# Optimization experiments

Measured on AMD Instinct MI355X. Metric: run time of the kernel, lower is better.

## Reference

```python
import jax, jax.numpy as jnp
import numpy as np

N = 100000   # nodes
E = 1600000  # directed edges
HID = 64


def gat_conv(x, src, dst, W, a_src, a_dst, b, heads, out_ch):
    """PyG-style GATConv (add_self_loops=True, negative_slope=0.2, concat)."""
    n = x.shape[0]
    h = (x @ W).reshape(n, heads, out_ch)              # [N,H,C]
    loop = jnp.arange(n, dtype=src.dtype)
    s = jnp.concatenate([src, loop])                   # self loops appended
    d = jnp.concatenate([dst, loop])
    alpha_src = jnp.sum(h * a_src, axis=-1)            # [N,H]
    alpha_dst = jnp.sum(h * a_dst, axis=-1)            # [N,H]
    alpha = jax.nn.leaky_relu(alpha_src[s] + alpha_dst[d], 0.2)  # [E+N,H]
    # segment softmax over incoming edges of each destination node
    amax = jax.ops.segment_max(alpha, d, num_segments=n)
    alpha = jnp.exp(alpha - amax[d])
    asum = jax.ops.segment_sum(alpha, d, num_segments=n)
    alpha = alpha / (asum[d] + 1e-16)
    msg = h[s] * alpha[:, :, None]                     # [E+N,H,C]
    out = jax.ops.segment_sum(msg, d, num_segments=n)  # [N,H,C]
    return out.reshape(n, heads * out_ch) + b


def setup_inputs() -> dict:
    key = jax.random.key(0)
    ks = jax.random.split(key, 22)
    rn = lambda k, shp, s=0.1: (jax.random.normal(k, shp, jnp.float32) * s)
    inp = {
        "x": jax.random.normal(ks[0], (N, 2), jnp.float32),
        "edge_index": jax.random.randint(ks[1], (2, E), 0, N, dtype=jnp.int32),
        "edge_attr": jax.random.normal(ks[2], (E, 2), jnp.float32),
        # node encoder
        "enc_W": rn(ks[3], (2, HID)), "enc_b": rn(ks[4], (HID,)),
        # gat1: heads=4, out=16
        "g1_W": rn(ks[5], (HID, HID)), "g1_as": rn(ks[6], (4, 16)),
        "g1_ad": rn(ks[7], (4, 16)), "g1_b": rn(ks[8], (HID,)),
        # gat2: heads=1, out=64
        "g2_W": rn(ks[9], (HID, HID)), "g2_as": rn(ks[10], (1, HID)),
        "g2_ad": rn(ks[11], (1, HID)), "g2_b": rn(ks[12], (HID,)),
        # node head
        "no_W1": rn(ks[13], (HID, HID)), "no_b1": rn(ks[14], (HID,)),
        "no_W2": rn(ks[15], (HID, 2)), "no_b2": rn(ks[16], (2,)),
        # edge head: in = 2*HID + 2 = 130
        "eo_W1": rn(ks[17], (2 * HID + 2, HID)), "eo_b1": rn(ks[18], (HID,)),
        "eo_W2": rn(ks[19], (HID, 1)), "eo_b2": rn(ks[20], (1,)),
    }
    return inp


def reference(x, edge_index, edge_attr, enc_W, enc_b,
              g1_W, g1_as, g1_ad, g1_b,
              g2_W, g2_as, g2_ad, g2_b,
              no_W1, no_b1, no_W2, no_b2,
              eo_W1, eo_b1, eo_W2, eo_b2):
    src, dst = edge_index[0], edge_index[1]
    h = x @ enc_W + enc_b                                    # node encoder (dropout = eval identity)
    h = jax.nn.elu(gat_conv(h, src, dst, g1_W, g1_as, g1_ad, g1_b, 4, 16))
    h = gat_conv(h, src, dst, g2_W, g2_as, g2_ad, g2_b, 1, HID)
    e_in = jnp.concatenate([h[src], h[dst], edge_attr], axis=-1)  # [E,130]
    node_pred = jnp.tanh(jax.nn.leaky_relu(h @ no_W1 + no_b1, 0.01) @ no_W2 + no_b2)
    edge_pred = jnp.tanh(jax.nn.leaky_relu(e_in @ eo_W1 + eo_b1, 0.01) @ eo_W2 + eo_b2)[:, 0]
    return edge_pred, node_pred
```

## Files before the change

kernel.cpp:

```cpp
#include <hip/hip_runtime.h>
#include <hip/hip_fp16.h>
#include <math.h>


typedef _Float16 half8_t __attribute__((ext_vector_type(8)));
typedef float floatx4 __attribute__((ext_vector_type(4)));

__global__ void k_scatter(const int* __restrict__ src, const int* __restrict__ dst,
                          int E, int NB, int cap, int* cursor,
                          unsigned int* __restrict__ ebuf,
                          const float* __restrict__ encW, const float* __restrict__ encb,
                          const float* __restrict__ g1W, float* __restrict__ Mc){
  __shared__ int hist[256];
  __shared__ int base[256];
  int t = threadIdx.x;
  if (blockIdx.x == 0 && t < 64){
    float m0 = 0.f, m1 = 0.f, cc = 0.f;
    for (int k = 0; k < 64; ++k){
      float g = g1W[k * 64 + t];
      m0 = fmaf(encW[k], g, m0);
      m1 = fmaf(encW[64 + k], g, m1);
      cc = fmaf(encb[k], g, cc);
    }
    Mc[t] = m0; Mc[64 + t] = m1; Mc[128 + t] = cc;
  }
  hist[t] = 0;
  __syncthreads();
  int cbase = blockIdx.x * 2048;
  int sv[8], bk[8], dl[8];
  #pragma unroll
  for (int i = 0; i < 8; ++i){
    int e = cbase + i * 256 + t;
    if (e < E){
      int d = dst[e];
      sv[i] = src[e]; bk[i] = d >> 9; dl[i] = d & 511;
      atomicAdd(&hist[bk[i]], 1);
    } else bk[i] = -1;
  }
  __syncthreads();
  int c = hist[t];
  base[t] = (t < NB && c > 0) ? (t * cap + atomicAdd(&cursor[t], c)) : 0;
  __syncthreads();
  hist[t] = 0;
  __syncthreads();
  #pragma unroll
  for (int i = 0; i < 8; ++i){
    if (bk[i] >= 0){
      int r = atomicAdd(&hist[bk[i]], 1);
      int p = base[bk[i]] + r;
      if (p < (bk[i] + 1) * cap)
        ebuf[p] = (unsigned)sv[i] | ((unsigned)dl[i] << 17);
    }
  }
}

__global__ void k_bucket_build(const int* __restrict__ cursor, int cap, int N,
                               unsigned int* ebuf, int* __restrict__ rstart,
                               int* __restrict__ rend,
                               const float* __restrict__ as4,
                               const float* __restrict__ ad4,
                               float4* __restrict__ palpha4){
  __shared__ unsigned int ent[12288];
  __shared__ int cnts[512];
  __shared__ int aux[512];
  int b = blockIdx.x, t = threadIdx.x;
  int base = b * cap;
  int cnt = cursor[b];
  if (cnt > cap) cnt = cap;
  for (int i = t; i < cnt; i += 512) ent[i] = ebuf[base + i];
  cnts[t] = 0;
  __syncthreads();
  for (int i = t; i < cnt; i += 512) atomicAdd(&cnts[ent[i] >> 17], 1);
  __syncthreads();
  int v = cnts[t];
  aux[t] = v;
  __syncthreads();
  for (int off = 1; off < 512; off <<= 1){
    int x = (t >= off) ? aux[t - off] : 0;
    __syncthreads();
    aux[t] += x;
    __syncthreads();
  }
  int incl = aux[t];
  int node = (b << 9) + t;
  if (node < N){ rstart[node] = base + incl - v; rend[node] = base + incl; }
  cnts[t] = incl - v;
  __syncthreads();
  for (int i = t; i < cnt; i += 512){
    unsigned int en = ent[i];
    int dl = en >> 17;
    int s = en & 0x1FFFFu;
    int pos = atomicAdd(&cnts[dl], 1);
    ebuf[base + pos] = en;
    int d = (b << 9) + dl;
    float4 sv = ((const float4*)as4)[s];
    float4 dv = ((const float4*)ad4)[d];
    float a0 = sv.x + dv.x, a1 = sv.y + dv.y, a2 = sv.z + dv.z, a3 = sv.w + dv.w;
    a0 = a0 > 0.f ? a0 : 0.2f * a0;
    a1 = a1 > 0.f ? a1 : 0.2f * a1;
    a2 = a2 > 0.f ? a2 : 0.2f * a2;
    a3 = a3 > 0.f ? a3 : 0.2f * a3;
    float4 pv = {__expf(a0), __expf(a1), __expf(a2), __expf(a3)};
    palpha4[base + pos] = pv;
  }
}

__global__ void k_palpha1(const int* __restrict__ cursor, int cap,
                          const unsigned int* __restrict__ ebuf,
                          const float* __restrict__ as, const float* __restrict__ ad,
                          float* __restrict__ palpha1){
  int blk = blockIdx.x;
  int b = blk >> 2, part = blk & 3;
  int base = b * cap;
  int cnt = cursor[b];
  if (cnt > cap) cnt = cap;
  for (int i = part * 256 + threadIdx.x; i < cnt; i += 1024){
    unsigned int en = ebuf[base + i];
    int s = en & 0x1FFFFu;
    int d = (b << 9) + (en >> 17);
    float a = as[s] + ad[d];
    a = a > 0.f ? a : 0.2f * a;
    palpha1[base + i] = __expf(a);
  }
}

__global__ void k_fuse1(const float* __restrict__ x, const float* __restrict__ Mc,
                        const float* __restrict__ a_s, const float* __restrict__ a_d,
                        __half* __restrict__ hw, float* __restrict__ alpha_s,
                        float* __restrict__ alpha_d, int n){
  int idx = blockIdx.x * blockDim.x + threadIdx.x;
  if (idx >= n * 64) return;
  int node = idx >> 6, j = idx & 63;
  float acc = fmaf(x[node * 2 + 0], Mc[j], fmaf(x[node * 2 + 1], Mc[64 + j], Mc[128 + j]));
  hw[idx] = __float2half(acc);
  float ps = acc * a_s[j];
  float pd = acc * a_d[j];
  #pragma unroll
  for (int off = 1; off < 16; off <<= 1){
    ps += __shfl_xor(ps, off);
    pd += __shfl_xor(pd, off);
  }
  if ((j & 15) == 0){
    int h = j >> 4;
    alpha_s[node * 4 + h] = ps;
    alpha_d[node * 4 + h] = pd;
  }
}

__global__ __launch_bounds__(256) void k_hw_mfma(
    const float* __restrict__ hin, const float* __restrict__ W,
    const float* __restrict__ a_s, const float* __restrict__ a_d,
    __half* __restrict__ hw, float* __restrict__ alpha_s,
    float* __restrict__ alpha_d, int n){
  __shared__ float redS[4][16];
  __shared__ float redD[4][16];
  int t = threadIdx.x;
  int lane = t & 63, wave = t >> 6;
  int l15 = lane & 15, quad = lane >> 4;
  int ch = wave * 16 + l15;
  half8_t b0, b1;
  #pragma unroll
  for (int j = 0; j < 8; ++j){
    b0[j] = (_Float16)W[(quad * 8 + j) * 64 + ch];
    b1[j] = (_Float16)W[(quad * 8 + j + 32) * 64 + ch];
  }
  float asv = a_s[ch], adv = a_d[ch];
  int base = blockIdx.x * 64;
  for (int it = 0; it < 4; ++it){
    int tb = base + it * 16;
    if (tb >= n) break;
    int arn = tb + l15; if (arn >= n) arn = n - 1;
    const float* arow = hin + (size_t)arn * 64 + quad * 8;
    half8_t a0, a1;
    #pragma unroll
    for (int j = 0; j < 8; ++j){
      a0[j] = (_Float16)arow[j];
      a1[j] = (_Float16)arow[j + 32];
    }
    floatx4 acc = {0.f, 0.f, 0.f, 0.f};
    acc = __builtin_amdgcn_mfma_f32_16x16x32_f16(a0, b0, acc, 0, 0, 0);
    acc = __builtin_amdgcn_mfma_f32_16x16x32_f16(a1, b1, acc, 0, 0, 0);
    float ps[4], pd[4];
    #pragma unroll
    for (int r = 0; r < 4; ++r){
      int node = tb + quad * 4 + r;
      if (node < n) hw[(size_t)node * 64 + ch] = __float2half(acc[r]);
      ps[r] = acc[r] * asv;
      pd[r] = acc[r] * adv;
      #pragma unroll
      for (int off = 1; off < 16; off <<= 1){
        ps[r] += __shfl_xor(ps[r], off);
        pd[r] += __shfl_xor(pd[r], off);
      }
    }
    if (l15 == 0){
      #pragma unroll
      for (int r = 0; r < 4; ++r){
        redS[wave][quad * 4 + r] = ps[r];
        redD[wave][quad * 4 + r] = pd[r];
      }
    }
    __syncthreads();
    if (t < 16 && tb + t < n){
      alpha_s[tb + t] = redS[0][t] + redS[1][t] + redS[2][t] + redS[3][t];
      alpha_d[tb + t] = redD[0][t] + redD[1][t] + redD[2][t] + redD[3][t];
    }
    __syncthreads();
  }
}

template<int H, bool ELU_ACT>
__global__ void k_agg(const __half* __restrict__ hw, const float* __restrict__ palpha,
                      const float* __restrict__ alpha_s, const float* __restrict__ alpha_d,
                      const int* __restrict__ rstart, const int* __restrict__ rend,
                      const unsigned int* __restrict__ ebuf,
                      const float* __restrict__ bias, float* __restrict__ hout, int n){
  int node = (blockIdx.x * blockDim.x + threadIdx.x) >> 6;
  int lane = threadIdx.x & 63;
  int g = lane >> 4, c = lane & 15;
  if (node >= n) return;
  int hidx = (c * H) >> 4;
  int start = rstart[node], end = rend[node];
  float acc0 = 0.f, acc1 = 0.f, acc2 = 0.f, acc3 = 0.f, psum = 0.f;
  if (g == 0){
    float a = alpha_s[node * H + hidx] + alpha_d[node * H + hidx];
    a = a > 0.f ? a : 0.2f * a;
    float p = __expf(a);
    psum = p;
    float2 rv = *(const float2*)(hw + (size_t)node * 64 + c * 4);
    const __half2* hp = (const __half2*)&rv;
    float2 f0 = __half22float2(hp[0]), f1 = __half22float2(hp[1]);
    acc0 = p * f0.x; acc1 = p * f0.y; acc2 = p * f1.x; acc3 = p * f1.y;
  }
  int i = start + g;
  for (; i + 4 < end; i += 8){
    int s0 = ebuf[i] & 0x1FFFF;
    int s1 = ebuf[i + 4] & 0x1FFFF;
    float p0 = palpha[(size_t)i * H + hidx];
    float p1 = palpha[(size_t)(i + 4) * H + hidx];
    float2 rv0 = *(const float2*)(hw + (size_t)s0 * 64 + c * 4);
    float2 rv1 = *(const float2*)(hw + (size_t)s1 * 64 + c * 4);
    const __half2* h0 = (const __half2*)&rv0;
    const __half2* h1 = (const __half2*)&rv1;
    float2 a0 = __half22float2(h0[0]), b0 = __half22float2(h0[1]);
    float2 a1 = __half22float2(h1[0]), b1 = __half22float2(h1[1]);
    psum += p0 + p1;
    acc0 = fmaf(p0, a0.x, fmaf(p1, a1.x, acc0));
    acc1 = fmaf(p0, a0.y, fmaf(p1, a1.y, acc1));
    acc2 = fmaf(p0, b0.x, fmaf(p1, b1.x, acc2));
    acc3 = fmaf(p0, b0.y, fmaf(p1, b1.y, acc3));
  }
  if (i < end){
    int s = ebuf[i] & 0x1FFFF;
    float p = palpha[(size_t)i * H + hidx];
    float2 rv = *(const float2*)(hw + (size_t)s * 64 + c * 4);
    const __half2* hp = (const __half2*)&rv;
    float2 f0 = __half22float2(hp[0]), f1 = __half22float2(hp[1]);
    psum += p;
    acc0 = fmaf(p, f0.x, acc0);
    acc1 = fmaf(p, f0.y, acc1);
    acc2 = fmaf(p, f1.x, acc2);
    acc3 = fmaf(p, f1.y, acc3);
  }
  #pragma unroll
  for (int off = 16; off < 64; off <<= 1){
    psum += __shfl_xor(psum, off);
    acc0 += __shfl_xor(acc0, off);
    acc1 += __shfl_xor(acc1, off);
    acc2 += __shfl_xor(acc2, off);
    acc3 += __shfl_xor(acc3, off);
  }
  if (g == 0){
    float inv = 1.f / (psum + 1e-16f);
    float4 bv = ((const float4*)bias)[c];
    float o0 = fmaf(acc0, inv, bv.x);
    float o1 = fmaf(acc1, inv, bv.y);
    float o2 = fmaf(acc2, inv, bv.z);
    float o3 = fmaf(acc3, inv, bv.w);
    if (ELU_ACT){
      o0 = o0 > 0.f ? o0 : (__expf(o0) - 1.f);
      o1 = o1 > 0.f ? o1 : (__expf(o1) - 1.f);
      o2 = o2 > 0.f ? o2 : (__expf(o2) - 1.f);
      o3 = o3 > 0.f ? o3 : (__expf(o3) - 1.f);
    }
    float4 ov = {o0, o1, o2, o3};
    *(float4*)(hout + (size_t)node * 64 + c * 4) = ov;
  }
}

__global__ __launch_bounds__(256) void k_heads_mfma(
    const float* __restrict__ h, const float* __restrict__ eoW1,
    const float* __restrict__ noW1, const float* __restrict__ nob1,
    const float* __restrict__ noW2, const float* __restrict__ nob2,
    __half* __restrict__ P1, __half* __restrict__ P2,
    float* __restrict__ outN, int n){
  __shared__ float redP[4][16][2];
  int t = threadIdx.x;
  int lane = t & 63, wave = t >> 6;
  int l15 = lane & 15, quad = lane >> 4;
  int ch = wave * 16 + l15;
  half8_t bP1a, bP1b, bP2a, bP2b, bNa, bNb;
  #pragma unroll
  for (int j = 0; j < 8; ++j){
    int k0 = quad * 8 + j, k1 = k0 + 32;
    bP1a[j] = (_Float16)eoW1[k0 * 64 + ch];
    bP1b[j] = (_Float16)eoW1[k1 * 64 + ch];
    bP2a[j] = (_Float16)eoW1[(k0 + 64) * 64 + ch];
    bP2b[j] = (_Float16)eoW1[(k1 + 64) * 64 + ch];
    bNa[j]  = (_Float16)noW1[k0 * 64 + ch];
    bNb[j]  = (_Float16)noW1[k1 * 64 + ch];
  }
  float b1v = nob1[ch];
  float w20 = noW2[ch * 2 + 0], w21 = noW2[ch * 2 + 1];
  float b20 = nob2[0], b21 = nob2[1];
  int base = blockIdx.x * 64;
  for (int it = 0; it < 4; ++it){
    int tb = base + it * 16;
    if (tb >= n) break;
    int arn = tb + l15; if (arn >= n) arn = n - 1;
    const float* arow = h + (size_t)arn * 64 + quad * 8;
    half8_t a0, a1;
    #pragma unroll
    for (int j = 0; j < 8; ++j){
      a0[j] = (_Float16)arow[j];
      a1[j] = (_Float16)arow[j + 32];
    }
    floatx4 ac1 = {0.f,0.f,0.f,0.f}, ac2 = {0.f,0.f,0.f,0.f}, acN = {0.f,0.f,0.f,0.f};
    ac1 = __builtin_amdgcn_mfma_f32_16x16x32_f16(a0, bP1a, ac1, 0, 0, 0);
    ac1 = __builtin_amdgcn_mfma_f32_16x16x32_f16(a1, bP1b, ac1, 0, 0, 0);
    ac2 = __builtin_amdgcn_mfma_f32_16x16x32_f16(a0, bP2a, ac2, 0, 0, 0);
    ac2 = __builtin_amdgcn_mfma_f32_16x16x32_f16(a1, bP2b, ac2, 0, 0, 0);
    acN = __builtin_amdgcn_mfma_f32_16x16x32_f16(a0, bNa, acN, 0, 0, 0);
    acN = __builtin_amdgcn_mfma_f32_16x16x32_f16(a1, bNb, acN, 0, 0, 0);
    float p0[4], p1[4];
    #pragma unroll
    for (int r = 0; r < 4; ++r){
      int node = tb + quad * 4 + r;
      if (node < n){
        P1[(size_t)node * 64 + ch] = __float2half(ac1[r]);
        P2[(size_t)node * 64 + ch] = __float2half(ac2[r]);
      }
      float v = acN[r] + b1v;
      v = v > 0.f ? v : 0.01f * v;
      p0[r] = v * w20;
      p1[r] = v * w21;
      #pragma unroll
      for (int off = 1; off < 16; off <<= 1){
        p0[r] += __shfl_xor(p0[r], off);
        p1[r] += __shfl_xor(p1[r], off);
      }
    }
    if (l15 == 0){
      #pragma unroll
      for (int r = 0; r < 4; ++r){
        redP[wave][quad * 4 + r][0] = p0[r];
        redP[wave][quad * 4 + r][1] = p1[r];
      }
    }
    __syncthreads();
    if (t < 16 && tb + t < n){
      float s0 = redP[0][t][0] + redP[1][t][0] + redP[2][t][0] + redP[3][t][0];
      float s1 = redP[0][t][1] + redP[1][t][1] + redP[2][t][1] + redP[3][t][1];
      outN[(size_t)(tb + t) * 2 + 0] = tanhf(s0 + b20);
      outN[(size_t)(tb + t) * 2 + 1] = tanhf(s1 + b21);
    }
    __syncthreads();
  }
}

__global__ void k_edge_head(const __half* __restrict__ P1h, const __half* __restrict__ P2h,
                            const int* __restrict__ src, const int* __restrict__ dst,
                            const float* __restrict__ eattr, const float* __restrict__ eoW1,
                            const float* __restrict__ b1, const float* __restrict__ W2,
                            const float* __restrict__ b2, float* __restrict__ out, int E){
  int lane = threadIdx.x & 63;
  int jj = lane & 7, q = lane >> 3;
  int wid = (blockIdx.x * blockDim.x + threadIdx.x) >> 6;
  int nw = (gridDim.x * blockDim.x) >> 6;

  const float4* rAq = (const float4*)(eoW1 + 8192);
  const float4* rBq = (const float4*)(eoW1 + 8256);
  const float4* b1q = (const float4*)b1;
  const float4* w2q = (const float4*)W2;
  float4 tA0 = rAq[2 * jj], tA1 = rAq[2 * jj + 1];
  float4 tB0 = rBq[2 * jj], tB1 = rBq[2 * jj + 1];
  float4 tb0 = b1q[2 * jj], tb1 = b1q[2 * jj + 1];
  float4 tw0 = w2q[2 * jj], tw1 = w2q[2 * jj + 1];
  float ra[8] = {tA0.x, tA0.y, tA0.z, tA0.w, tA1.x, tA1.y, tA1.z, tA1.w};
  float rb[8] = {tB0.x, tB0.y, tB0.z, tB0.w, tB1.x, tB1.y, tB1.z, tB1.w};
  float bb[8] = {tb0.x, tb0.y, tb0.z, tb0.w, tb1.x, tb1.y, tb1.z, tb1.w};
  float w2[8] = {tw0.x, tw0.y, tw0.z, tw0.w, tw1.x, tw1.y, tw1.z, tw1.w};
  float b2v = b2[0];

  const float4* P1q = (const float4*)P1h;
  const float4* P2q = (const float4*)P2h;
  const float2* eav = (const float2*)eattr;

  int groups = (E + 7) >> 3;
  for (int g = wid; g < groups; g += nw){
    int e = g * 8 + q;
    bool act = (e < E);
    float p = 0.f;
    if (act){
      int s = src[e], d = dst[e];
      float2 ea = eav[e];
      float4 g1 = P1q[(size_t)s * 8 + jj];
      float4 g2 = P2q[(size_t)d * 8 + jj];
      const __half2* h1 = (const __half2*)&g1;
      const __half2* h2 = (const __half2*)&g2;
      float v[8];
      #pragma unroll
      for (int k = 0; k < 4; ++k){
        float2 u = __half22float2(h1[k]);
        float2 w = __half22float2(h2[k]);
        v[2 * k]     = u.x + w.x;
        v[2 * k + 1] = u.y + w.y;
      }
      #pragma unroll
      for (int k = 0; k < 8; ++k){
        float t = v[k] + bb[k];
        t = fmaf(ea.x, ra[k], fmaf(ea.y, rb[k], t));
        t = t > 0.f ? t : 0.01f * t;
        p = fmaf(t, w2[k], p);
      }
    }
    #pragma unroll
    for (int off = 1; off < 8; off <<= 1) p += __shfl_xor(p, off);
    if (jj == 0 && act) out[e] = tanhf(p + b2v);
  }
}

extern "C" void kernel_launch(void* const* d_in, const int* in_sizes, int n_in,
                              void* d_out, int out_size, void* d_ws, size_t ws_size,
                              hipStream_t stream){
  const float* x    = (const float*)d_in[0];
  const int*   eidx = (const int*)  d_in[1];
  const float* ea   = (const float*)d_in[2];
  const float* encW = (const float*)d_in[3];
  const float* encb = (const float*)d_in[4];
  const float* g1W  = (const float*)d_in[5];
  const float* g1as = (const float*)d_in[6];
  const float* g1ad = (const float*)d_in[7];
  const float* g1b  = (const float*)d_in[8];
  const float* g2W  = (const float*)d_in[9];
  const float* g2as = (const float*)d_in[10];
  const float* g2ad = (const float*)d_in[11];
  const float* g2b  = (const float*)d_in[12];
  const float* noW1 = (const float*)d_in[13];
  const float* nob1 = (const float*)d_in[14];
  const float* noW2 = (const float*)d_in[15];
  const float* nob2 = (const float*)d_in[16];
  const float* eoW1 = (const float*)d_in[17];
  const float* eob1 = (const float*)d_in[18];
  const float* eoW2 = (const float*)d_in[19];
  const float* eob2 = (const float*)d_in[20];

  const int N = in_sizes[0] / 2;
  const int E = in_sizes[1] / 2;
  const int* src = eidx;
  const int* dst = eidx + E;

  const int NB = (N + 511) >> 9;
  int avg = (E + NB - 1) / NB;
  int cap = avg + avg / 4 + 64;
  if (cap > 12288) cap = 12288;

  char* ws = (char*)d_ws;
  size_t off = 0;
  auto alloc = [&](size_t bytes) -> void* {
    void* p = ws + off;
    off = (off + bytes + 255) & ~(size_t)255;
    return p;
  };
  float*  bufA  = (float*) alloc((size_t)N * 64 * 4);
  __half* bufH  = (__half*)alloc((size_t)N * 64 * 2);
  __half* P1h   = (__half*)alloc((size_t)N * 64 * 2);
  __half* P2h   = (__half*)alloc((size_t)N * 64 * 2);
  float*  as    = (float*) alloc((size_t)N * 4 * 4);
  float*  ad    = (float*) alloc((size_t)N * 4 * 4);
  int* rstart   = (int*)   alloc((size_t)N * 4);
  int* rend     = (int*)   alloc((size_t)N * 4);
  unsigned int* ebuf = (unsigned int*)alloc((size_t)NB * cap * 4);
  float4* palpha4 = (float4*)alloc((size_t)NB * cap * 16);
  float* palpha1  = (float*)palpha4;
  int* cursor   = (int*)   alloc((size_t)NB * 4);
  float* Mc     = (float*) alloc(192 * 4);

  hipMemsetAsync(cursor, 0, (size_t)NB * 4, stream);
  k_scatter<<<(E + 2047) / 2048, 256, 0, stream>>>(src, dst, E, NB, cap, cursor, ebuf,
                                                   encW, encb, g1W, Mc);
  k_fuse1<<<(N * 64 + 255) / 256, 256, 0, stream>>>(x, Mc, g1as, g1ad, bufH, as, ad, N);
  k_bucket_build<<<NB, 512, 0, stream>>>(cursor, cap, N, ebuf, rstart, rend, as, ad, palpha4);
  k_agg<4, true><<<(N + 3) / 4, 256, 0, stream>>>(bufH, (const float*)palpha4, as, ad,
                                                  rstart, rend, ebuf, g1b, bufA, N);
  k_hw_mfma<<<(N + 63) / 64, 256, 0, stream>>>(bufA, g2W, g2as, g2ad, bufH, as, ad, N);
  k_palpha1<<<NB * 4, 256, 0, stream>>>(cursor, cap, ebuf, as, ad, palpha1);
  k_agg<1, false><<<(N + 3) / 4, 256, 0, stream>>>(bufH, palpha1, as, ad,
                                                   rstart, rend, ebuf, g2b, bufA, N);
  float* out = (float*)d_out;
  k_heads_mfma<<<(N + 63) / 64, 256, 0, stream>>>(bufA, eoW1, noW1, nob1, noW2, nob2,
                                                  P1h, P2h, out + E, N);
  k_edge_head<<<2048, 256, 0, stream>>>(P1h, P2h, src, dst, ea,
                                        eoW1, eob1, eoW2, eob2, out, E);
}
```

Before: 402.1 us.

## Split layer-1 alpha out of bucket build, widen agg lanes, unroll edge head

Layer-1 edge attention exponentials move out of the bucket-build kernel into a templated k_palpha kernel shared with layer 2, which keeps the bucket-build kernel light. The aggregation kernel now has each lane own 8 channels with 16-byte loads, so 8 edges are processed per wavefront step instead of 4, which increases memory-level parallelism on the gather. The edge-head kernel handles two edges per group to expose more independent loads. The cost is one extra kernel launch and a second pass over ebuf, plus more registers in the aggregation kernel.

```diff
diff --git a/kernel.cpp b/kernel.cpp
--- a/kernel.cpp
+++ b/kernel.cpp
@@ -56,10 +56,7 @@
 
 __global__ void k_bucket_build(const int* __restrict__ cursor, int cap, int N,
                                unsigned int* ebuf, int* __restrict__ rstart,
-                               int* __restrict__ rend,
-                               const float* __restrict__ as4,
-                               const float* __restrict__ ad4,
-                               float4* __restrict__ palpha4){
+                               int* __restrict__ rend){
   __shared__ unsigned int ent[12288];
   __shared__ int cnts[512];
   __shared__ int aux[512];
@@ -88,27 +85,16 @@
   __syncthreads();
   for (int i = t; i < cnt; i += 512){
     unsigned int en = ent[i];
-    int dl = en >> 17;
-    int s = en & 0x1FFFFu;
-    int pos = atomicAdd(&cnts[dl], 1);
+    int pos = atomicAdd(&cnts[en >> 17], 1);
     ebuf[base + pos] = en;
-    int d = (b << 9) + dl;
-    float4 sv = ((const float4*)as4)[s];
-    float4 dv = ((const float4*)ad4)[d];
-    float a0 = sv.x + dv.x, a1 = sv.y + dv.y, a2 = sv.z + dv.z, a3 = sv.w + dv.w;
-    a0 = a0 > 0.f ? a0 : 0.2f * a0;
-    a1 = a1 > 0.f ? a1 : 0.2f * a1;
-    a2 = a2 > 0.f ? a2 : 0.2f * a2;
-    a3 = a3 > 0.f ? a3 : 0.2f * a3;
-    float4 pv = {__expf(a0), __expf(a1), __expf(a2), __expf(a3)};
-    palpha4[base + pos] = pv;
-  }
-}
-
-__global__ void k_palpha1(const int* __restrict__ cursor, int cap,
-                          const unsigned int* __restrict__ ebuf,
-                          const float* __restrict__ as, const float* __restrict__ ad,
-                          float* __restrict__ palpha1){
+  }
+}
+
+template<int H>
+__global__ void k_palpha(const int* __restrict__ cursor, int cap,
+                         const unsigned int* __restrict__ ebuf,
+                         const float* __restrict__ as, const float* __restrict__ ad,
+                         float* __restrict__ palpha){
   int blk = blockIdx.x;
   int b = blk >> 2, part = blk & 3;
   int base = b * cap;
@@ -118,9 +104,21 @@
     unsigned int en = ebuf[base + i];
     int s = en & 0x1FFFFu;
     int d = (b << 9) + (en >> 17);
-    float a = as[s] + ad[d];
-    a = a > 0.f ? a : 0.2f * a;
-    palpha1[base + i] = __expf(a);
+    if (H == 4){
+      float4 sv = ((const float4*)as)[s];
+      float4 dv = ((const float4*)ad)[d];
+      float a0 = sv.x + dv.x, a1 = sv.y + dv.y, a2 = sv.z + dv.z, a3 = sv.w + dv.w;
+      a0 = a0 > 0.f ? a0 : 0.2f * a0;
+      a1 = a1 > 0.f ? a1 : 0.2f * a1;
+      a2 = a2 > 0.f ? a2 : 0.2f * a2;
+      a3 = a3 > 0.f ? a3 : 0.2f * a3;
+      float4 pv = {__expf(a0), __expf(a1), __expf(a2), __expf(a3)};
+      ((float4*)palpha)[base + i] = pv;
+    } else {
+      float a = as[s] + ad[d];
+      a = a > 0.f ? a : 0.2f * a;
+      palpha[base + i] = __expf(a);
+    }
   }
 }
 
@@ -217,74 +215,82 @@
                       const float* __restrict__ bias, float* __restrict__ hout, int n){
   int node = (blockIdx.x * blockDim.x + threadIdx.x) >> 6;
   int lane = threadIdx.x & 63;
-  int g = lane >> 4, c = lane & 15;
+  int g = lane >> 3, jj = lane & 7;
   if (node >= n) return;
-  int hidx = (c * H) >> 4;
+  int hidx = (jj * H) >> 3;
   int start = rstart[node], end = rend[node];
-  float acc0 = 0.f, acc1 = 0.f, acc2 = 0.f, acc3 = 0.f, psum = 0.f;
+  float acc[8] = {0.f,0.f,0.f,0.f,0.f,0.f,0.f,0.f};
+  float psum = 0.f;
   if (g == 0){
     float a = alpha_s[node * H + hidx] + alpha_d[node * H + hidx];
     a = a > 0.f ? a : 0.2f * a;
     float p = __expf(a);
     psum = p;
-    float2 rv = *(const float2*)(hw + (size_t)node * 64 + c * 4);
+    float4 rv = *(const float4*)(hw + (size_t)node * 64 + jj * 8);
     const __half2* hp = (const __half2*)&rv;
-    float2 f0 = __half22float2(hp[0]), f1 = __half22float2(hp[1]);
-    acc0 = p * f0.x; acc1 = p * f0.y; acc2 = p * f1.x; acc3 = p * f1.y;
+    #pragma unroll
+    for (int k = 0; k < 4; ++k){
+      float2 f = __half22float2(hp[k]);
+      acc[2 * k] = p * f.x; acc[2 * k + 1] = p * f.y;
+    }
   }
   int i = start + g;
-  for (; i + 4 < end; i += 8){
-    int s0 = ebuf[i] & 0x1FFFF;
-    int s1 = ebuf[i + 4] & 0x1FFFF;
+  for (; i + 8 < end; i += 16){
+    unsigned int e0 = ebuf[i], e1 = ebuf[i + 8];
+    int s0 = e0 & 0x1FFFF, s1 = e1 & 0x1FFFF;
     float p0 = palpha[(size_t)i * H + hidx];
-    float p1 = palpha[(size_t)(i + 4) * H + hidx];
-    float2 rv0 = *(const float2*)(hw + (size_t)s0 * 64 + c * 4);
-    float2 rv1 = *(const float2*)(hw + (size_t)s1 * 64 + c * 4);
-    const __half2* h0 = (const __half2*)&rv0;
-    const __half2* h1 = (const __half2*)&rv1;
-    float2 a0 = __half22float2(h0[0]), b0 = __half22float2(h0[1]);
-    float2 a1 = __half22float2(h1[0]), b1 = __half22float2(h1[1]);
+    float p1 = palpha[(size_t)(i + 8) * H + hidx];
+    float4 r0 = *(const float4*)(hw + (size_t)s0 * 64 + jj * 8);
+    float4 r1 = *(const float4*)(hw + (size_t)s1 * 64 + jj * 8);
+    const __half2* h0 = (const __half2*)&r0;
+    const __half2* h1 = (const __half2*)&r1;
     psum += p0 + p1;
-    acc0 = fmaf(p0, a0.x, fmaf(p1, a1.x, acc0));
-    acc1 = fmaf(p0, a0.y, fmaf(p1, a1.y, acc1));
-    acc2 = fmaf(p0, b0.x, fmaf(p1, b1.x, acc2));
-    acc3 = fmaf(p0, b0.y, fmaf(p1, b1.y, acc3));
+    #pragma unroll
+    for (int k = 0; k < 4; ++k){
+      float2 f0 = __half22float2(h0[k]);
+      float2 f1 = __half22float2(h1[k]);
+      acc[2 * k]     = fmaf(p0, f0.x, fmaf(p1, f1.x, acc[2 * k]));
+      acc[2 * k + 1] = fmaf(p0, f0.y, fmaf(p1, f1.y, acc[2 * k + 1]));
+    }
   }
   if (i < end){
-    int s = ebuf[i] & 0x1FFFF;
+    unsigned int en = ebuf[i];
+    int s = en & 0x1FFFF;
     float p = palpha[(size_t)i * H + hidx];
-    float2 rv = *(const float2*)(hw + (size_t)s * 64 + c * 4);
+    float4 rv = *(const float4*)(hw + (size_t)s * 64 + jj * 8);
     const __half2* hp = (const __half2*)&rv;
-    float2 f0 = __half22float2(hp[0]), f1 = __half22float2(hp[1]);
     psum += p;
-    acc0 = fmaf(p, f0.x, acc0);
-    acc1 = fmaf(p, f0.y, acc1);
-    acc2 = fmaf(p, f1.x, acc2);
-    acc3 = fmaf(p, f1.y, acc3);
+    #pragma unroll
+    for (int k = 0; k < 4; ++k){
+      float2 f = __half22float2(hp[k]);
+      acc[2 * k]     = fmaf(p, f.x, acc[2 * k]);
+      acc[2 * k + 1] = fmaf(p, f.y, acc[2 * k + 1]);
+    }
   }
   #pragma unroll
-  for (int off = 16; off < 64; off <<= 1){
+  for (int off = 8; off < 64; off <<= 1){
     psum += __shfl_xor(psum, off);
-    acc0 += __shfl_xor(acc0, off);
-    acc1 += __shfl_xor(acc1, off);
-    acc2 += __shfl_xor(acc2, off);
-    acc3 += __shfl_xor(acc3, off);
+    #pragma unroll
+    for (int k = 0; k < 8; ++k) acc[k] += __shfl_xor(acc[k], off);
   }
   if (g == 0){
     float inv = 1.f / (psum + 1e-16f);
-    float4 bv = ((const float4*)bias)[c];
-    float o0 = fmaf(acc0, inv, bv.x);
-    float o1 = fmaf(acc1, inv, bv.y);
-    float o2 = fmaf(acc2, inv, bv.z);
-    float o3 = fmaf(acc3, inv, bv.w);
+    float4 bv0 = ((const float4*)bias)[2 * jj];
+    float4 bv1 = ((const float4*)bias)[2 * jj + 1];
+    float o[8];
+    o[0] = fmaf(acc[0], inv, bv0.x); o[1] = fmaf(acc[1], inv, bv0.y);
+    o[2] = fmaf(acc[2], inv, bv0.z); o[3] = fmaf(acc[3], inv, bv0.w);
+    o[4] = fmaf(acc[4], inv, bv1.x); o[5] = fmaf(acc[5], inv, bv1.y);
+    o[6] = fmaf(acc[6], inv, bv1.z); o[7] = fmaf(acc[7], inv, bv1.w);
     if (ELU_ACT){
-      o0 = o0 > 0.f ? o0 : (__expf(o0) - 1.f);
-      o1 = o1 > 0.f ? o1 : (__expf(o1) - 1.f);
-      o2 = o2 > 0.f ? o2 : (__expf(o2) - 1.f);
-      o3 = o3 > 0.f ? o3 : (__expf(o3) - 1.f);
-    }
-    float4 ov = {o0, o1, o2, o3};
-    *(float4*)(hout + (size_t)node * 64 + c * 4) = ov;
+      #pragma unroll
+      for (int k = 0; k < 8; ++k) o[k] = o[k] > 0.f ? o[k] : (__expf(o[k]) - 1.f);
+    }
+    float4 ov0 = {o[0], o[1], o[2], o[3]};
+    float4 ov1 = {o[4], o[5], o[6], o[7]};
+    float* dstp = hout + (size_t)node * 64 + jj * 8;
+    *(float4*)dstp = ov0;
+    *(float4*)(dstp + 4) = ov1;
   }
 }
 
@@ -396,37 +402,60 @@
   const float4* P2q = (const float4*)P2h;
   const float2* eav = (const float2*)eattr;
 
-  int groups = (E + 7) >> 3;
+  int groups = (E + 15) >> 4;
   for (int g = wid; g < groups; g += nw){
-    int e = g * 8 + q;
-    bool act = (e < E);
-    float p = 0.f;
-    if (act){
-      int s = src[e], d = dst[e];
-      float2 ea = eav[e];
+    int e0 = g * 16 + q, e1 = e0 + 8;
+    bool act0 = (e0 < E), act1 = (e1 < E);
+    float p0 = 0.f, p1 = 0.f;
+    if (act0){
+      int s = src[e0], d = dst[e0];
+      float2 ea = eav[e0];
       float4 g1 = P1q[(size_t)s * 8 + jj];
       float4 g2 = P2q[(size_t)d * 8 + jj];
       const __half2* h1 = (const __half2*)&g1;
       const __half2* h2 = (const __half2*)&g2;
-      float v[8];
       #pragma unroll
       for (int k = 0; k < 4; ++k){
         float2 u = __half22float2(h1[k]);
         float2 w = __half22float2(h2[k]);
-        v[2 * k]     = u.x + w.x;
-        v[2 * k + 1] = u.y + w.y;
-      }
-      #pragma unroll
-      for (int k = 0; k < 8; ++k){
-        float t = v[k] + bb[k];
-        t = fmaf(ea.x, ra[k], fmaf(ea.y, rb[k], t));
-        t = t > 0.f ? t : 0.01f * t;
-        p = fmaf(t, w2[k], p);
-      }
-    }
-    #pragma unroll
-    for (int off = 1; off < 8; off <<= 1) p += __shfl_xor(p, off);
-    if (jj == 0 && act) out[e] = tanhf(p + b2v);
+        float ta = u.x + w.x + bb[2 * k];
+        float tb = u.y + w.y + bb[2 * k + 1];
+        ta = fmaf(ea.x, ra[2 * k], fmaf(ea.y, rb[2 * k], ta));
+        tb = fmaf(ea.x, ra[2 * k + 1], fmaf(ea.y, rb[2 * k + 1], tb));
+        ta = ta > 0.f ? ta : 0.01f * ta;
+        tb = tb > 0.f ? tb : 0.01f * tb;
+        p0 = fmaf(ta, w2[2 * k], fmaf(tb, w2[2 * k + 1], p0));
+      }
+    }
+    if (act1){
+      int s = src[e1], d = dst[e1];
+      float2 ea = eav[e1];
+      float4 g1 = P1q[(size_t)s * 8 + jj];
+      float4 g2 = P2q[(size_t)d * 8 + jj];
+      const __half2* h1 = (const __half2*)&g1;
+      const __half2* h2 = (const __half2*)&g2;
+      #pragma unroll
+      for (int k = 0; k < 4; ++k){
+        float2 u = __half22float2(h1[k]);
+        float2 w = __half22float2(h2[k]);
+        float ta = u.x + w.x + bb[2 * k];
+        float tb = u.y + w.y + bb[2 * k + 1];
+        ta = fmaf(ea.x, ra[2 * k], fmaf(ea.y, rb[2 * k], ta));
+        tb = fmaf(ea.x, ra[2 * k + 1], fmaf(ea.y, rb[2 * k + 1], tb));
+        ta = ta > 0.f ? ta : 0.01f * ta;
+        tb = tb > 0.f ? tb : 0.01f * tb;
+        p1 = fmaf(ta, w2[2 * k], fmaf(tb, w2[2 * k + 1], p1));
+      }
+    }
+    #pragma unroll
+    for (int off = 1; off < 8; off <<= 1){
+      p0 += __shfl_xor(p0, off);
+      p1 += __shfl_xor(p1, off);
+    }
+    if (jj == 0){
+      if (act0) out[e0] = tanhf(p0 + b2v);
+      if (act1) out[e1] = tanhf(p1 + b2v);
+    }
   }
 }
 
@@ -481,8 +510,7 @@
   int* rstart   = (int*)   alloc((size_t)N * 4);
   int* rend     = (int*)   alloc((size_t)N * 4);
   unsigned int* ebuf = (unsigned int*)alloc((size_t)NB * cap * 4);
-  float4* palpha4 = (float4*)alloc((size_t)NB * cap * 16);
-  float* palpha1  = (float*)palpha4;
+  float* palphaB = (float*)alloc((size_t)NB * cap * 16);
   int* cursor   = (int*)   alloc((size_t)NB * 4);
   float* Mc     = (float*) alloc(192 * 4);
 
@@ -490,12 +518,13 @@
   k_scatter<<<(E + 2047) / 2048, 256, 0, stream>>>(src, dst, E, NB, cap, cursor, ebuf,
                                                    encW, encb, g1W, Mc);
   k_fuse1<<<(N * 64 + 255) / 256, 256, 0, stream>>>(x, Mc, g1as, g1ad, bufH, as, ad, N);
-  k_bucket_build<<<NB, 512, 0, stream>>>(cursor, cap, N, ebuf, rstart, rend, as, ad, palpha4);
-  k_agg<4, true><<<(N + 3) / 4, 256, 0, stream>>>(bufH, (const float*)palpha4, as, ad,
+  k_bucket_build<<<NB, 512, 0, stream>>>(cursor, cap, N, ebuf, rstart, rend);
+  k_palpha<4><<<NB * 4, 256, 0, stream>>>(cursor, cap, ebuf, as, ad, palphaB);
+  k_agg<4, true><<<(N + 3) / 4, 256, 0, stream>>>(bufH, palphaB, as, ad,
                                                   rstart, rend, ebuf, g1b, bufA, N);
   k_hw_mfma<<<(N + 63) / 64, 256, 0, stream>>>(bufA, g2W, g2as, g2ad, bufH, as, ad, N);
-  k_palpha1<<<NB * 4, 256, 0, stream>>>(cursor, cap, ebuf, as, ad, palpha1);
-  k_agg<1, false><<<(N + 3) / 4, 256, 0, stream>>>(bufH, palpha1, as, ad,
+  k_palpha<1><<<NB * 4, 256, 0, stream>>>(cursor, cap, ebuf, as, ad, palphaB);
+  k_agg<1, false><<<(N + 3) / 4, 256, 0, stream>>>(bufH, palphaB, as, ad,
                                                    rstart, rend, ebuf, g2b, bufA, N);
   float* out = (float*)d_out;
   k_heads_mfma<<<(N + 63) / 64, 256, 0, stream>>>(bufA, eoW1, noW1, nob1, noW2, nob2,
```

Result: faster. 384.5 us (-4.4%).
